# Optimization experiments

Measured on AMD Instinct MI355X. Metric: run time of the kernel, lower is better.

The kernel has to match this reference:

```python
import jax, jax.numpy as jnp
import numpy as np

N, E = 50000, 800000
IN_CH, OUT_CH, HEADS, EDGE_DIM = 128, 32, 4, 16
OUT_TOTAL = OUT_CH * HEADS  # 128 == IN_CH -> skip is Identity
NEG_SLOPE = 0.2
BN_EPS = 1e-5


def setup_inputs() -> dict:
    key = jax.random.key(0)
    ks = jax.random.split(key, 12)
    s = 1.0 / np.sqrt(IN_CH)
    return {
        "x": jax.random.normal(ks[0], (N, IN_CH), jnp.float32),
        "edge_index": jax.random.randint(ks[1], (2, E), 0, N, jnp.int64),
        "edge_attr": jax.random.normal(ks[2], (E, EDGE_DIM), jnp.float32),
        # GATv2Conv params (share_weights=False): lin_l, lin_r, lin_edge, att, bias
        "W_l": jax.random.uniform(ks[3], (IN_CH, OUT_TOTAL), jnp.float32, -s, s),
        "W_r": jax.random.uniform(ks[4], (IN_CH, OUT_TOTAL), jnp.float32, -s, s),
        "W_e": jax.random.uniform(ks[5], (EDGE_DIM, OUT_TOTAL), jnp.float32, -0.25, 0.25),
        "att": jax.random.uniform(ks[6], (HEADS, OUT_CH), jnp.float32, -s, s),
        "bias": jnp.zeros((OUT_TOTAL,), jnp.float32),
        "bn_gamma": jnp.ones((OUT_TOTAL,), jnp.float32),
        "bn_beta": jnp.zeros((OUT_TOTAL,), jnp.float32),
    }


def reference(x, edge_index, edge_attr, W_l, W_r, W_e, att, bias, bn_gamma, bn_beta):
    src, dst = edge_index[0], edge_index[1]
    # GATv2Conv: per-node linear projections, reshaped to [N, H, C]
    xl = (x @ W_l).reshape(N, HEADS, OUT_CH)
    xr = (x @ W_r).reshape(N, HEADS, OUT_CH)
    # edge-wise attention input: x_l[src] + x_r[dst] + lin_edge(edge_attr)
    e = xl[src] + xr[dst] + (edge_attr @ W_e).reshape(E, HEADS, OUT_CH)
    e = jax.nn.leaky_relu(e, NEG_SLOPE)
    score = jnp.einsum('ehc,hc->eh', e, att)  # [E, H]
    # segment softmax over destination nodes
    smax = jax.ops.segment_max(score, dst, num_segments=N)
    ex = jnp.exp(score - smax[dst])
    denom = jax.ops.segment_sum(ex, dst, num_segments=N)
    alpha = ex / denom[dst]  # [E, H]
    # weighted scatter-aggregation of source features
    msg = xl[src] * alpha[:, :, None]  # [E, H, C]
    out = jax.ops.segment_sum(msg, dst, num_segments=N).reshape(N, OUT_TOTAL) + bias
    # BatchNorm1d (training-mode batch stats, biased variance)
    mu = out.mean(axis=0)
    var = out.var(axis=0)
    out = (out - mu) * jax.lax.rsqrt(var + BN_EPS) * bn_gamma + bn_beta
    out = jax.nn.elu(out)
    # dropout: eval -> identity; skip: Identity (in_channels == out_total)
    return out + x
```

## Files before the change

kernel.cpp:

```cpp
#include <hip/hip_runtime.h>
#include <math.h>

#define N_NODES 50000
#define E_EDGES 800000
#define NEG_SLOPE 0.2f
#define BN_EPS 1e-5f
#define NWAVES 8192
#define LDB 132
#define NB_SCAN 196
#define NB_PROJ 782
#define NB_CNT 3125

using bf4 = __attribute__((ext_vector_type(4))) short;
using bf8 = __attribute__((ext_vector_type(8))) short;
using f32x4 = __attribute__((ext_vector_type(4))) float;
using half2v = __attribute__((ext_vector_type(2))) _Float16;

__device__ __forceinline__ unsigned short f2b(float f) {
  unsigned u = __float_as_uint(f);
  return (unsigned short)((u + 0x7FFFu + ((u >> 16) & 1u)) >> 16);
}
__device__ __forceinline__ float b2f_lo(unsigned u) {
  return __uint_as_float(u << 16);
}
__device__ __forceinline__ float b2f_hi(unsigned u) {
  return __uint_as_float(u & 0xFFFF0000u);
}

__global__ __launch_bounds__(256) void k_projcnt(
    const float* __restrict__ x, const float* __restrict__ Wl,
    const float* __restrict__ Wr, unsigned short* __restrict__ xlb,
    unsigned short* __restrict__ xrb, const int* __restrict__ ei,
    const float* __restrict__ ea, int* __restrict__ deg,
    int4* __restrict__ eah) {
  const int t = threadIdx.x;

  if (blockIdx.x >= NB_PROJ) {
    int e = (blockIdx.x - NB_PROJ) * 256 + t;
    if (e >= E_EDGES) return;
    atomicAdd(&deg[ei[E_EDGES + e]], 1);
    const float4* r = (const float4*)(ea + (size_t)e * 16);
    float4 v0 = r[0], v1 = r[1], v2 = r[2], v3 = r[3];
    union {
      half2v h[8];
      int4 q[2];
    } u;
    u.h[0] = (half2v){(_Float16)v0.x, (_Float16)v0.y};
    u.h[1] = (half2v){(_Float16)v0.z, (_Float16)v0.w};
    u.h[2] = (half2v){(_Float16)v1.x, (_Float16)v1.y};
    u.h[3] = (half2v){(_Float16)v1.z, (_Float16)v1.w};
    u.h[4] = (half2v){(_Float16)v2.x, (_Float16)v2.y};
    u.h[5] = (half2v){(_Float16)v2.z, (_Float16)v2.w};
    u.h[6] = (half2v){(_Float16)v3.x, (_Float16)v3.y};
    u.h[7] = (half2v){(_Float16)v3.z, (_Float16)v3.w};
    eah[(size_t)e * 2] = u.q[0];
    eah[(size_t)e * 2 + 1] = u.q[1];
    return;
  }

  __shared__ __align__(16) unsigned short blds[256 * LDB];
#pragma unroll
  for (int s = 0; s < 32; ++s) {
    int i4 = s * 256 + t;
    int k = (i4 * 4) >> 8;
    int colb = (i4 * 4) & 255;
    float4 w = (colb < 128) ? *(const float4*)(Wl + k * 128 + colb)
                            : *(const float4*)(Wr + k * 128 + (colb - 128));
    blds[(colb + 0) * LDB + k] = f2b(w.x);
    blds[(colb + 1) * LDB + k] = f2b(w.y);
    blds[(colb + 2) * LDB + k] = f2b(w.z);
    blds[(colb + 3) * LDB + k] = f2b(w.w);
  }
  __syncthreads();

  const int wave = t >> 6, lane = t & 63;
  const int f = lane & 15;
  const int g = lane >> 4;
  const int r0 = blockIdx.x * 64 + wave * 16;
  const int row = r0 + f;
  const bool rok = row < N_NODES;

  f32x4 acc[16];
#pragma unroll
  for (int c = 0; c < 16; ++c) acc[c] = (f32x4){0.f, 0.f, 0.f, 0.f};

#pragma unroll
  for (int ks = 0; ks < 4; ++ks) {
    bf8 a;
    if (rok) {
      const float* ap = x + (size_t)row * 128 + ks * 32 + g * 8;
      float4 a0 = *(const float4*)(ap);
      float4 a1 = *(const float4*)(ap + 4);
      a = (bf8){(short)f2b(a0.x), (short)f2b(a0.y), (short)f2b(a0.z),
                (short)f2b(a0.w), (short)f2b(a1.x), (short)f2b(a1.y),
                (short)f2b(a1.z), (short)f2b(a1.w)};
    } else {
      a = (bf8){0, 0, 0, 0, 0, 0, 0, 0};
    }
#pragma unroll
    for (int c = 0; c < 16; ++c) {
      const bf4* bp =
          (const bf4*)(blds + (c * 16 + f) * LDB + ks * 32 + g * 8);
      bf8 b = __builtin_shufflevector(bp[0], bp[1], 0, 1, 2, 3, 4, 5, 6, 7);
      acc[c] = __builtin_amdgcn_mfma_f32_16x16x32_bf16(a, b, acc[c], 0, 0, 0);
    }
  }

#pragma unroll
  for (int c = 0; c < 16; ++c) {
    unsigned short* dst = (c < 8) ? xlb : xrb;
    int cc = (c * 16 + f) & 127;
#pragma unroll
    for (int r = 0; r < 4; ++r) {
      int rr = r0 + g * 4 + r;
      if (rr < N_NODES) dst[(size_t)rr * 128 + cc] = f2b(acc[c][r]);
    }
  }
}

__global__ __launch_bounds__(256) void k_scan_blk(const int* __restrict__ deg,
                                                  int* __restrict__ offs,
                                                  int* __restrict__ bsum) {
  __shared__ int s[256];
  int t = threadIdx.x, idx = blockIdx.x * 256 + t;
  int v = (idx < N_NODES) ? deg[idx] : 0;
  s[t] = v;
  __syncthreads();
  int acc = v;
#pragma unroll
  for (int off = 1; off < 256; off <<= 1) {
    int u = (t >= off) ? s[t - off] : 0;
    __syncthreads();
    acc += u;
    s[t] = acc;
    __syncthreads();
  }
  if (idx < N_NODES) offs[idx] = acc - v;
  if (t == 255) bsum[blockIdx.x] = acc;
}

__global__ __launch_bounds__(256) void k_scan_top(int* __restrict__ bsum) {
  __shared__ int s[256];
  int t = threadIdx.x;
  int v = (t < NB_SCAN) ? bsum[t] : 0;
  s[t] = v;
  __syncthreads();
  int acc = v;
#pragma unroll
  for (int off = 1; off < 256; off <<= 1) {
    int u = (t >= off) ? s[t - off] : 0;
    __syncthreads();
    acc += u;
    s[t] = acc;
    __syncthreads();
  }
  if (t < NB_SCAN) bsum[t] = acc - v;
}

__global__ __launch_bounds__(256) void k_scan_add(int* __restrict__ offs,
                                                  const int* __restrict__ bsum) {
  int idx = blockIdx.x * 256 + threadIdx.x;
  if (idx < N_NODES) offs[idx] += bsum[blockIdx.x];
}

__global__ __launch_bounds__(256) void k_fill(const int* __restrict__ ei,
                                              const int* __restrict__ offs,
                                              int* __restrict__ cur,
                                              int2* __restrict__ se) {
  int e = blockIdx.x * 256 + threadIdx.x;
  if (e >= E_EDGES) return;
  int d = ei[E_EDGES + e];
  int p = offs[d] + atomicAdd(&cur[d], 1);
  se[p] = make_int2(ei[e], e);
}

__device__ __forceinline__ float fscore16(const half2v* eav,
                                          const half2v* we0h,
                                          const half2v* we1h, float xrx,
                                          float xry, float ax, float ay,
                                          float xlx, float xly) {
  float xe0 = 0.f, xe1 = 0.f;
#pragma unroll
  for (int k = 0; k < 8; ++k) {
#if __has_builtin(__builtin_amdgcn_fdot2)
    xe0 = __builtin_amdgcn_fdot2(eav[k], we0h[k], xe0, false);
    xe1 = __builtin_amdgcn_fdot2(eav[k], we1h[k], xe1, false);
#else
    xe0 += (float)eav[k][0] * (float)we0h[k][0] +
           (float)eav[k][1] * (float)we0h[k][1];
    xe1 += (float)eav[k][0] * (float)we1h[k][0] +
           (float)eav[k][1] * (float)we1h[k][1];
#endif
  }
  float v0 = xlx + xrx + xe0;
  float v1 = xly + xry + xe1;
  v0 = v0 > 0.f ? v0 : NEG_SLOPE * v0;
  v1 = v1 > 0.f ? v1 : NEG_SLOPE * v1;
  float p = v0 * ax + v1 * ay;
  p += __shfl_xor(p, 1);
  p += __shfl_xor(p, 2);
  p += __shfl_xor(p, 4);
  p += __shfl_xor(p, 8);
  return p;
}

#define UPD(p, xx, xy)              \
  {                                 \
    float mn = fmaxf(m, (p));       \
    float sc = __expf(m - mn);      \
    float pe = __expf((p)-mn);      \
    den = den * sc + pe;            \
    a0 = a0 * sc + pe * (xx);       \
    a1 = a1 * sc + pe * (xy);       \
    m = mn;                         \
  }

__global__ __launch_bounds__(256, 8) void k_node(
    const unsigned short* __restrict__ xlb,
    const unsigned short* __restrict__ xrb, const int2* __restrict__ se,
    const int4* __restrict__ eah, const float* __restrict__ We,
    const float* __restrict__ att, const int* __restrict__ offs,
    const int* __restrict__ deg, float* __restrict__ out) {
  const int wid = __builtin_amdgcn_readfirstlane(
      (int)((blockIdx.x * 256 + threadIdx.x) >> 6));
  const int lane = threadIdx.x & 63;
  const int c0 = lane * 2;

  half2v we0h[8], we1h[8];
#pragma unroll
  for (int j = 0; j < 8; ++j) {
    float2 wa = *(const float2*)(We + (2 * j) * 128 + c0);
    float2 wb = *(const float2*)(We + (2 * j + 1) * 128 + c0);
    we0h[j] = (half2v){(_Float16)wa.x, (_Float16)wb.x};
    we1h[j] = (half2v){(_Float16)wa.y, (_Float16)wb.y};
  }
  float2 aw = *(const float2*)(att + c0);

  for (int d = wid; d < N_NODES; d += NWAVES) {
    const int base = __builtin_amdgcn_readfirstlane(offs[d]);
    const int n = __builtin_amdgcn_readfirstlane(deg[d]);
    unsigned ur = *(const unsigned*)(xrb + (size_t)d * 128 + c0);
    float xrx = b2f_lo(ur), xry = b2f_hi(ur);

    float m = -INFINITY, den = 0.f, a0 = 0.f, a1 = 0.f;
    int i = 0;
    for (; i + 4 <= n; i += 4) {
      int2 q0 = se[base + i];
      int2 q1 = se[base + i + 1];
      int2 q2 = se[base + i + 2];
      int2 q3 = se[base + i + 3];
      int s0 = __builtin_amdgcn_readfirstlane(q0.x);
      int s1 = __builtin_amdgcn_readfirstlane(q1.x);
      int s2 = __builtin_amdgcn_readfirstlane(q2.x);
      int s3 = __builtin_amdgcn_readfirstlane(q3.x);
      int e0 = __builtin_amdgcn_readfirstlane(q0.y);
      int e1 = __builtin_amdgcn_readfirstlane(q1.y);
      int e2 = __builtin_amdgcn_readfirstlane(q2.y);
      int e3 = __builtin_amdgcn_readfirstlane(q3.y);
      union {
        int4 q[8];
        half2v h[32];
      } u;
      u.q[0] = eah[(size_t)e0 * 2];
      u.q[1] = eah[(size_t)e0 * 2 + 1];
      u.q[2] = eah[(size_t)e1 * 2];
      u.q[3] = eah[(size_t)e1 * 2 + 1];
      u.q[4] = eah[(size_t)e2 * 2];
      u.q[5] = eah[(size_t)e2 * 2 + 1];
      u.q[6] = eah[(size_t)e3 * 2];
      u.q[7] = eah[(size_t)e3 * 2 + 1];
      unsigned uA = *(const unsigned*)(xlb + (size_t)s0 * 128 + c0);
      unsigned uB = *(const unsigned*)(xlb + (size_t)s1 * 128 + c0);
      unsigned uC = *(const unsigned*)(xlb + (size_t)s2 * 128 + c0);
      unsigned uD = *(const unsigned*)(xlb + (size_t)s3 * 128 + c0);
      float xAx = b2f_lo(uA), xAy = b2f_hi(uA);
      float xBx = b2f_lo(uB), xBy = b2f_hi(uB);
      float xCx = b2f_lo(uC), xCy = b2f_hi(uC);
      float xDx = b2f_lo(uD), xDy = b2f_hi(uD);
      float pA = fscore16(u.h, we0h, we1h, xrx, xry, aw.x, aw.y, xAx, xAy);
      float pB =
          fscore16(u.h + 8, we0h, we1h, xrx, xry, aw.x, aw.y, xBx, xBy);
      float pC =
          fscore16(u.h + 16, we0h, we1h, xrx, xry, aw.x, aw.y, xCx, xCy);
      float pD =
          fscore16(u.h + 24, we0h, we1h, xrx, xry, aw.x, aw.y, xDx, xDy);
      UPD(pA, xAx, xAy);
      UPD(pB, xBx, xBy);
      UPD(pC, xCx, xCy);
      UPD(pD, xDx, xDy);
    }
    for (; i < n; ++i) {
      int2 q = se[base + i];
      int s0 = __builtin_amdgcn_readfirstlane(q.x);
      int e0 = __builtin_amdgcn_readfirstlane(q.y);
      union {
        int4 q[2];
        half2v h[8];
      } u;
      u.q[0] = eah[(size_t)e0 * 2];
      u.q[1] = eah[(size_t)e0 * 2 + 1];
      unsigned uv = *(const unsigned*)(xlb + (size_t)s0 * 128 + c0);
      float xx = b2f_lo(uv), xy = b2f_hi(uv);
      float p = fscore16(u.h, we0h, we1h, xrx, xry, aw.x, aw.y, xx, xy);
      UPD(p, xx, xy);
    }

    float inv = (n > 0) ? 1.f / den : 0.f;
    float2 o;
    o.x = a0 * inv;
    o.y = a1 * inv;
    *(float2*)(out + (size_t)d * 128 + c0) = o;
  }
}

__global__ __launch_bounds__(256) void k_bnstat(const float* __restrict__ out,
                                                float* __restrict__ bnsum,
                                                float* __restrict__ bnsq) {
  __shared__ float ls[256][4];
  __shared__ float lq[256][4];
  int t = threadIdx.x;
  int cg = t & 31;
  int rg = t >> 5;
  float s0 = 0, s1 = 0, s2 = 0, s3 = 0, q0 = 0, q1 = 0, q2 = 0, q3 = 0;
  for (int r = blockIdx.x * 8 + rg; r < N_NODES; r += gridDim.x * 8) {
    float4 v = ((const float4*)out)[(size_t)r * 32 + cg];
    s0 += v.x; s1 += v.y; s2 += v.z; s3 += v.w;
    q0 += v.x * v.x; q1 += v.y * v.y; q2 += v.z * v.z; q3 += v.w * v.w;
  }
  ls[t][0] = s0; ls[t][1] = s1; ls[t][2] = s2; ls[t][3] = s3;
  lq[t][0] = q0; lq[t][1] = q1; lq[t][2] = q2; lq[t][3] = q3;
  __syncthreads();
  if (t < 32) {
#pragma unroll
    for (int g = 1; g < 8; ++g) {
#pragma unroll
      for (int i = 0; i < 4; ++i) {
        ls[t][i] += ls[g * 32 + t][i];
        lq[t][i] += lq[g * 32 + t][i];
      }
    }
#pragma unroll
    for (int i = 0; i < 4; ++i) {
      unsafeAtomicAdd(bnsum + 4 * t + i, ls[t][i]);
      unsafeAtomicAdd(bnsq + 4 * t + i, lq[t][i]);
    }
  }
}

__global__ __launch_bounds__(256) void k_final(
    const float* __restrict__ agg, const float* __restrict__ x,
    const float* __restrict__ bnsum, const float* __restrict__ bnsq,
    const float* __restrict__ gamma, const float* __restrict__ beta,
    float* __restrict__ out) {
  __shared__ __align__(16) float ssc[128];
  __shared__ __align__(16) float ssh[128];
  int t = threadIdx.x;
  if (t < 128) {
    float mu = bnsum[t] * (1.0f / N_NODES);
    float var = bnsq[t] * (1.0f / N_NODES) - mu * mu;
    float sc = gamma[t] * rsqrtf(var + BN_EPS);
    ssc[t] = sc;
    ssh[t] = beta[t] - mu * sc;
  }
  __syncthreads();
  int i4 = blockIdx.x * 256 + t;
  if (i4 >= N_NODES * 32) return;
  int cbase = (i4 * 4) & 127;
  float4 v = ((const float4*)agg)[i4];
  float4 xv = ((const float4*)x)[i4];
  float4 sc = *(const float4*)(ssc + cbase);
  float4 sh = *(const float4*)(ssh + cbase);
  float r0 = v.x * sc.x + sh.x;
  float r1 = v.y * sc.y + sh.y;
  float r2 = v.z * sc.z + sh.z;
  float r3 = v.w * sc.w + sh.w;
  r0 = r0 > 0.f ? r0 : expm1f(r0);
  r1 = r1 > 0.f ? r1 : expm1f(r1);
  r2 = r2 > 0.f ? r2 : expm1f(r2);
  r3 = r3 > 0.f ? r3 : expm1f(r3);
  float4 o;
  o.x = r0 + xv.x; o.y = r1 + xv.y; o.z = r2 + xv.z; o.w = r3 + xv.w;
  ((float4*)out)[i4] = o;
}

extern "C" void kernel_launch(void* const* d_in, const int* in_sizes, int n_in,
                              void* d_out, int out_size, void* d_ws,
                              size_t ws_size, hipStream_t stream) {
  const float* x = (const float*)d_in[0];
  const int* ei = (const int*)d_in[1];
  const float* ea = (const float*)d_in[2];
  const float* Wl = (const float*)d_in[3];
  const float* Wr = (const float*)d_in[4];
  const float* We = (const float*)d_in[5];
  const float* att = (const float*)d_in[6];
  const float* gamma = (const float*)d_in[8];
  const float* beta = (const float*)d_in[9];
  float* out = (float*)d_out;

  unsigned short* xlb = (unsigned short*)d_ws;
  unsigned short* xrb = xlb + (size_t)N_NODES * 128;
  int* deg = (int*)(xrb + (size_t)N_NODES * 128);
  int* offs = deg + N_NODES;
  int* cur = offs + N_NODES;
  int* bsum = cur + N_NODES;
  int2* se = (int2*)(bsum + 256);
  int4* eah = (int4*)(se + E_EDGES);
  float* bnsum = (float*)(eah + (size_t)E_EDGES * 2);
  float* bnsq = bnsum + 128;

  hipMemsetAsync(deg, 0, 3 * N_NODES * sizeof(int), stream);
  hipMemsetAsync(bnsum, 0, 2 * 128 * sizeof(float), stream);

  k_projcnt<<<NB_PROJ + NB_CNT, 256, 0, stream>>>(x, Wl, Wr, xlb, xrb, ei, ea,
                                                  deg, eah);
  k_scan_blk<<<NB_SCAN, 256, 0, stream>>>(deg, offs, bsum);
  k_scan_top<<<1, 256, 0, stream>>>(bsum);
  k_scan_add<<<NB_SCAN, 256, 0, stream>>>(offs, bsum);
  k_fill<<<(E_EDGES + 255) / 256, 256, 0, stream>>>(ei, offs, cur, se);
  k_node<<<NWAVES / 4, 256, 0, stream>>>(xlb, xrb, se, eah, We, att, offs,
                                         deg, out);
  k_bnstat<<<256, 256, 0, stream>>>(out, bnsum, bnsq);
  k_final<<<(N_NODES * 32 + 255) / 256, 256, 0, stream>>>(out, x, bnsum, bnsq,
                                                          gamma, beta, out);
}
```

Before: 257.5 us.

## Merge scan and BN stat/final kernels into cooperative grid-sync launches

Measured after the change: 463.6 us. +80.0%, slower.

```diff
diff --git a/kernel.cpp b/kernel.cpp
--- a/kernel.cpp
+++ b/kernel.cpp
@@ -1,5 +1,8 @@
 #include <hip/hip_runtime.h>
+#include <hip/hip_cooperative_groups.h>
 #include <math.h>
+
+namespace cgrp = cooperative_groups;
 
 #define N_NODES 50000
 #define E_EDGES 800000
@@ -10,6 +13,7 @@
 #define NB_SCAN 196
 #define NB_PROJ 782
 #define NB_CNT 3125
+#define NB_BNF 1024
 
 using bf4 = __attribute__((ext_vector_type(4))) short;
 using bf8 = __attribute__((ext_vector_type(8))) short;
@@ -118,11 +122,16 @@
   }
 }
 
-__global__ __launch_bounds__(256) void k_scan_blk(const int* __restrict__ deg,
-                                                  int* __restrict__ offs,
-                                                  int* __restrict__ bsum) {
+__global__ __launch_bounds__(256) void k_scan_coop(const int* __restrict__ deg,
+                                                   int* __restrict__ offs,
+                                                   int* __restrict__ bsum,
+                                                   float* __restrict__ bn0) {
+  cgrp::grid_group grid = cgrp::this_grid();
   __shared__ int s[256];
-  int t = threadIdx.x, idx = blockIdx.x * 256 + t;
+  const int t = threadIdx.x;
+  const int idx = blockIdx.x * 256 + t;
+  if (blockIdx.x == 0) bn0[t] = 0.f;
+
   int v = (idx < N_NODES) ? deg[idx] : 0;
   s[t] = v;
   __syncthreads();
@@ -137,29 +146,27 @@
   }
   if (idx < N_NODES) offs[idx] = acc - v;
   if (t == 255) bsum[blockIdx.x] = acc;
-}
-
-__global__ __launch_bounds__(256) void k_scan_top(int* __restrict__ bsum) {
-  __shared__ int s[256];
-  int t = threadIdx.x;
-  int v = (t < NB_SCAN) ? bsum[t] : 0;
-  s[t] = v;
-  __syncthreads();
-  int acc = v;
-#pragma unroll
-  for (int off = 1; off < 256; off <<= 1) {
-    int u = (t >= off) ? s[t - off] : 0;
+
+  grid.sync();
+
+  if (blockIdx.x == 0) {
+    int bv = (t < NB_SCAN) ? bsum[t] : 0;
+    s[t] = bv;
     __syncthreads();
-    acc += u;
-    s[t] = acc;
-    __syncthreads();
-  }
-  if (t < NB_SCAN) bsum[t] = acc - v;
-}
-
-__global__ __launch_bounds__(256) void k_scan_add(int* __restrict__ offs,
-                                                  const int* __restrict__ bsum) {
-  int idx = blockIdx.x * 256 + threadIdx.x;
+    int bacc = bv;
+#pragma unroll
+    for (int off = 1; off < 256; off <<= 1) {
+      int u = (t >= off) ? s[t - off] : 0;
+      __syncthreads();
+      bacc += u;
+      s[t] = bacc;
+      __syncthreads();
+    }
+    if (t < NB_SCAN) bsum[t] = bacc - bv;
+  }
+
+  grid.sync();
+
   if (idx < N_NODES) offs[idx] += bsum[blockIdx.x];
 }
 
@@ -313,17 +320,22 @@
   }
 }
 
-__global__ __launch_bounds__(256) void k_bnstat(const float* __restrict__ out,
-                                                float* __restrict__ bnsum,
-                                                float* __restrict__ bnsq) {
+__global__ __launch_bounds__(256) void k_bnfinal(
+    const float* __restrict__ agg, const float* __restrict__ x,
+    float* __restrict__ bnsum, float* __restrict__ bnsq,
+    const float* __restrict__ gamma, const float* __restrict__ beta,
+    float* __restrict__ out) {
+  cgrp::grid_group grid = cgrp::this_grid();
   __shared__ float ls[256][4];
   __shared__ float lq[256][4];
-  int t = threadIdx.x;
-  int cg = t & 31;
-  int rg = t >> 5;
+  __shared__ __align__(16) float ssc[128];
+  __shared__ __align__(16) float ssh[128];
+  const int t = threadIdx.x;
+  const int cg_ = t & 31;
+  const int rg = t >> 5;
   float s0 = 0, s1 = 0, s2 = 0, s3 = 0, q0 = 0, q1 = 0, q2 = 0, q3 = 0;
-  for (int r = blockIdx.x * 8 + rg; r < N_NODES; r += gridDim.x * 8) {
-    float4 v = ((const float4*)out)[(size_t)r * 32 + cg];
+  for (int r = blockIdx.x * 8 + rg; r < N_NODES; r += NB_BNF * 8) {
+    float4 v = ((const float4*)agg)[(size_t)r * 32 + cg_];
     s0 += v.x; s1 += v.y; s2 += v.z; s3 += v.w;
     q0 += v.x * v.x; q1 += v.y * v.y; q2 += v.z * v.z; q3 += v.w * v.w;
   }
@@ -345,16 +357,9 @@
       unsafeAtomicAdd(bnsq + 4 * t + i, lq[t][i]);
     }
   }
-}
-
-__global__ __launch_bounds__(256) void k_final(
-    const float* __restrict__ agg, const float* __restrict__ x,
-    const float* __restrict__ bnsum, const float* __restrict__ bnsq,
-    const float* __restrict__ gamma, const float* __restrict__ beta,
-    float* __restrict__ out) {
-  __shared__ __align__(16) float ssc[128];
-  __shared__ __align__(16) float ssh[128];
-  int t = threadIdx.x;
+  __threadfence();
+  grid.sync();
+
   if (t < 128) {
     float mu = bnsum[t] * (1.0f / N_NODES);
     float var = bnsq[t] * (1.0f / N_NODES) - mu * mu;
@@ -363,24 +368,24 @@
     ssh[t] = beta[t] - mu * sc;
   }
   __syncthreads();
-  int i4 = blockIdx.x * 256 + t;
-  if (i4 >= N_NODES * 32) return;
-  int cbase = (i4 * 4) & 127;
-  float4 v = ((const float4*)agg)[i4];
-  float4 xv = ((const float4*)x)[i4];
-  float4 sc = *(const float4*)(ssc + cbase);
-  float4 sh = *(const float4*)(ssh + cbase);
-  float r0 = v.x * sc.x + sh.x;
-  float r1 = v.y * sc.y + sh.y;
-  float r2 = v.z * sc.z + sh.z;
-  float r3 = v.w * sc.w + sh.w;
-  r0 = r0 > 0.f ? r0 : expm1f(r0);
-  r1 = r1 > 0.f ? r1 : expm1f(r1);
-  r2 = r2 > 0.f ? r2 : expm1f(r2);
-  r3 = r3 > 0.f ? r3 : expm1f(r3);
-  float4 o;
-  o.x = r0 + xv.x; o.y = r1 + xv.y; o.z = r2 + xv.z; o.w = r3 + xv.w;
-  ((float4*)out)[i4] = o;
+  for (int i4 = blockIdx.x * 256 + t; i4 < N_NODES * 32; i4 += NB_BNF * 256) {
+    int cbase = (i4 * 4) & 127;
+    float4 v = ((const float4*)agg)[i4];
+    float4 xv = ((const float4*)x)[i4];
+    float4 sc = *(const float4*)(ssc + cbase);
+    float4 sh = *(const float4*)(ssh + cbase);
+    float r0 = v.x * sc.x + sh.x;
+    float r1 = v.y * sc.y + sh.y;
+    float r2 = v.z * sc.z + sh.z;
+    float r3 = v.w * sc.w + sh.w;
+    r0 = r0 > 0.f ? r0 : expm1f(r0);
+    r1 = r1 > 0.f ? r1 : expm1f(r1);
+    r2 = r2 > 0.f ? r2 : expm1f(r2);
+    r3 = r3 > 0.f ? r3 : expm1f(r3);
+    float4 o;
+    o.x = r0 + xv.x; o.y = r1 + xv.y; o.z = r2 + xv.z; o.w = r3 + xv.w;
+    ((float4*)out)[i4] = o;
+  }
 }
 
 extern "C" void kernel_launch(void* const* d_in, const int* in_sizes, int n_in,
@@ -409,17 +414,24 @@
   float* bnsq = bnsum + 128;
 
   hipMemsetAsync(deg, 0, 3 * N_NODES * sizeof(int), stream);
-  hipMemsetAsync(bnsum, 0, 2 * 128 * sizeof(float), stream);
 
   k_projcnt<<<NB_PROJ + NB_CNT, 256, 0, stream>>>(x, Wl, Wr, xlb, xrb, ei, ea,
                                                   deg, eah);
-  k_scan_blk<<<NB_SCAN, 256, 0, stream>>>(deg, offs, bsum);
-  k_scan_top<<<1, 256, 0, stream>>>(bsum);
-  k_scan_add<<<NB_SCAN, 256, 0, stream>>>(offs, bsum);
+
+  {
+    void* args[] = {(void*)&deg, (void*)&offs, (void*)&bsum, (void*)&bnsum};
+    hipLaunchCooperativeKernel((void*)k_scan_coop, dim3(NB_SCAN), dim3(256),
+                               args, 0, stream);
+  }
+
   k_fill<<<(E_EDGES + 255) / 256, 256, 0, stream>>>(ei, offs, cur, se);
   k_node<<<NWAVES / 4, 256, 0, stream>>>(xlb, xrb, se, eah, We, att, offs,
                                          deg, out);
-  k_bnstat<<<256, 256, 0, stream>>>(out, bnsum, bnsq);
-  k_final<<<(N_NODES * 32 + 255) / 256, 256, 0, stream>>>(out, x, bnsum, bnsq,
-                                                          gamma, beta, out);
-}
+
+  {
+    void* args[] = {(void*)&out,   (void*)&x,    (void*)&bnsum, (void*)&bnsq,
+                    (void*)&gamma, (void*)&beta, (void*)&out};
+    hipLaunchCooperativeKernel((void*)k_bnfinal, dim3(NB_BNF), dim3(256),
+                               args, 0, stream);
+  }
+}
```
